# Performance work log

Measured on AMD Instinct MI355X. Metric: run time of the kernel, lower is better.

## Reference

```python
import jax, jax.numpy as jnp
import numpy as np

NG, NC, FG, FC, D = 8192, 4096, 512, 256, 64
ALPHA = 0.2          # leaky_relu negative slope
NEG = -9.0e15        # mask fill value from the torch code


def _leaky(x):
    return jnp.where(x >= 0, x, ALPHA * x)


def _relation(h_src, h_dst, a, adj):
    # additive GAT score: e[i,j] = leaky(h_src[i]@a[:D] + h_dst[j]@a[D:])
    s1 = h_src @ a[:D]            # [Ns]
    s2 = h_dst @ a[D:]            # [Nd]
    e = _leaky(s1[:, None] + s2[None, :])          # [Ns, Nd]
    att = jax.nn.softmax(jnp.where(adj > 0, e, NEG), axis=1)
    return att @ h_dst            # [Ns, D]


def setup_inputs() -> dict:
    key = jax.random.key(0)
    ks = jax.random.split(key, 14)
    sc = 0.05
    return {
        "gene_x": jax.random.normal(ks[0], (NG, FG), jnp.float32),
        "cell_x": jax.random.normal(ks[1], (NC, FC), jnp.float32),
        "W_g": jax.random.normal(ks[2], (FG, D), jnp.float32) * sc,
        "W_c": jax.random.normal(ks[3], (FC, D), jnp.float32) * sc,
        "a_gg": jax.random.normal(ks[4], (2 * D,), jnp.float32) * sc,
        "a_gc": jax.random.normal(ks[5], (2 * D,), jnp.float32) * sc,
        "a_cc": jax.random.normal(ks[6], (2 * D,), jnp.float32) * sc,
        "a_cg": jax.random.normal(ks[7], (2 * D,), jnp.float32) * sc,
        "Wgate_g": jax.random.normal(ks[8], (D, 1), jnp.float32) * sc,
        "bgate_g": jnp.full((1,), -2.0, jnp.float32),
        "Wgate_c": jax.random.normal(ks[9], (D, 1), jnp.float32) * sc,
        "bgate_c": jnp.full((1,), -2.0, jnp.float32),
        "gene_adj": jax.random.randint(ks[10], (NG, NG), 0, 2, jnp.int32),
        "cell_adj": jax.random.randint(ks[11], (NC, NC), 0, 2, jnp.int32),
        "gene_cell_adj": jax.random.randint(ks[12], (NG, NC), 0, 2, jnp.int32),
    }


def reference(gene_x, cell_x, W_g, W_c, a_gg, a_gc, a_cc, a_cg,
              Wgate_g, bgate_g, Wgate_c, bgate_c,
              gene_adj, cell_adj, gene_cell_adj):
    gene_h = gene_x @ W_g                              # [NG, D]
    cell_h = cell_x @ W_c                              # [NC, D]

    gene_from_gene = _relation(gene_h, gene_h, a_gg, gene_adj)
    gene_from_cell = _relation(gene_h, cell_h, a_gc, gene_cell_adj)
    cell_from_cell = _relation(cell_h, cell_h, a_cc, cell_adj)
    cell_from_gene = _relation(cell_h, gene_h, a_cg, gene_cell_adj.T)

    gamma_g = jax.nn.sigmoid(gene_h @ Wgate_g + bgate_g)   # [NG, 1]
    gamma_c = jax.nn.sigmoid(cell_h @ Wgate_c + bgate_c)   # [NC, 1]

    gene_out = _leaky(gene_h + gene_from_gene + gamma_g * gene_from_cell)
    cell_out = _leaky(cell_h + cell_from_cell + gamma_c * cell_from_gene)
    return gene_out, cell_out
```

## Files before the change

### kernel.cpp

```cpp
#include <hip/hip_runtime.h>

#define NG 8192
#define NC 4096
#define FG 512
#define FC 256
#define ALPHA 0.2f

typedef float f32x4 __attribute__((ext_vector_type(4)));
typedef short bf16x8 __attribute__((ext_vector_type(8)));

static __device__ __forceinline__ float leakyf(float x) { return fmaxf(x, ALPHA * x); }

static __device__ __forceinline__ unsigned short f2bf(float f) {
    unsigned u = __builtin_bit_cast(unsigned, f);
    u += 0x7fffu + ((u >> 16) & 1u);
    return (unsigned short)(u >> 16);
}

static __device__ __forceinline__ float wred(float v) {
#pragma unroll
    for (int m = 1; m < 64; m <<= 1) v += __shfl_xor(v, m, 64);
    return v;
}

__global__ __launch_bounds__(256) void pack_all(
    const int* __restrict__ gene_adj, const int* __restrict__ cell_adj,
    const int* __restrict__ gc_adj,
    unsigned char* __restrict__ bmGG, unsigned char* __restrict__ bmCC,
    unsigned char* __restrict__ bmGC)
{
    const int wave = threadIdx.x >> 6, lane = threadIdx.x & 63;
    const int r = blockIdx.x * 4 + wave;
    const int* row; unsigned char* brow; int C;
    if (r < NG)           { row = gene_adj + (size_t)r * NG;              brow = bmGG + (size_t)r * (NG >> 3);              C = NG; }
    else if (r < NG + NC) { int rr = r - NG;      row = cell_adj + (size_t)rr * NC; brow = bmCC + (size_t)rr * (NC >> 3); C = NC; }
    else                  { int rr = r - NG - NC; row = gc_adj   + (size_t)rr * NC; brow = bmGC + (size_t)rr * (NC >> 3); C = NC; }
    for (int j = lane * 8; j < C; j += 512) {
        int4 a0 = *(const int4*)(row + j);
        int4 a1 = *(const int4*)(row + j + 4);
        unsigned b = (unsigned)(a0.x > 0)        | ((unsigned)(a0.y > 0) << 1)
                   | ((unsigned)(a0.z > 0) << 2) | ((unsigned)(a0.w > 0) << 3)
                   | ((unsigned)(a1.x > 0) << 4) | ((unsigned)(a1.y > 0) << 5)
                   | ((unsigned)(a1.z > 0) << 6) | ((unsigned)(a1.w > 0) << 7);
        brow[j >> 3] = (unsigned char)b;
    }
}

static __device__ __forceinline__ void proj_body(
    const float* __restrict__ x, const float* __restrict__ W, int K, int N,
    float* __restrict__ h, unsigned short* __restrict__ hT,
    const float* __restrict__ aA, const float* __restrict__ aB,
    const float* __restrict__ aC, const float* __restrict__ aD,
    const float* __restrict__ aG, const float* __restrict__ bG,
    float* __restrict__ sA, float* __restrict__ sB, float* __restrict__ sC,
    float* __restrict__ sD, float* __restrict__ gam, int blk)
{
    const int wave = threadIdx.x >> 6, lane = threadIdx.x & 63;
    const int r0 = blk * 16 + wave * 4;
    const float* xr = x + (size_t)r0 * K;
    float acc0 = 0.f, acc1 = 0.f, acc2 = 0.f, acc3 = 0.f;
    for (int k = 0; k < K; k += 4) {
        float4 x0 = *(const float4*)(xr + k);
        float4 x1 = *(const float4*)(xr + K + k);
        float4 x2 = *(const float4*)(xr + 2 * (size_t)K + k);
        float4 x3 = *(const float4*)(xr + 3 * (size_t)K + k);
        float w0 = W[(k + 0) * 64 + lane];
        float w1 = W[(k + 1) * 64 + lane];
        float w2 = W[(k + 2) * 64 + lane];
        float w3 = W[(k + 3) * 64 + lane];
        acc0 += x0.x * w0 + x0.y * w1 + x0.z * w2 + x0.w * w3;
        acc1 += x1.x * w0 + x1.y * w1 + x1.z * w2 + x1.w * w3;
        acc2 += x2.x * w0 + x2.y * w1 + x2.z * w2 + x2.w * w3;
        acc3 += x3.x * w0 + x3.y * w1 + x3.z * w2 + x3.w * w3;
    }
    float accs[4] = {acc0, acc1, acc2, acc3};
    unsigned short hb[4];
#pragma unroll
    for (int t = 0; t < 4; t++) {
        h[(size_t)(r0 + t) * 64 + lane] = accs[t];
        hb[t] = f2bf(accs[t]);
    }
    *(ushort4*)&hT[(size_t)lane * N + r0] = make_ushort4(hb[0], hb[1], hb[2], hb[3]);

    const float cA = aA[lane], cB = aB[lane], cC = aC[lane], cD = aD[lane], cG = aG[lane];
    const float bias = bG[0];
#pragma unroll
    for (int t = 0; t < 4; t++) {
        float vA = wred(accs[t] * cA);
        float vB = wred(accs[t] * cB);
        float vC = wred(accs[t] * cC);
        float vD = wred(accs[t] * cD);
        float vG = wred(accs[t] * cG);
        if (lane == 0) {
            sA[r0 + t] = vA; sB[r0 + t] = vB; sC[r0 + t] = vC; sD[r0 + t] = vD;
            gam[r0 + t] = 1.f / (1.f + __expf(-(vG + bias)));
        }
    }
}

__global__ __launch_bounds__(256) void proj_all(
    const float* __restrict__ gene_x, const float* __restrict__ W_g,
    const float* __restrict__ cell_x, const float* __restrict__ W_c,
    float* __restrict__ gene_h, unsigned short* __restrict__ gene_hT,
    float* __restrict__ cell_h, unsigned short* __restrict__ cell_hT,
    const float* __restrict__ a_gg, const float* __restrict__ a_gc,
    const float* __restrict__ a_cc, const float* __restrict__ a_cg,
    const float* __restrict__ Wgg, const float* __restrict__ bgg,
    const float* __restrict__ Wgc, const float* __restrict__ bgc,
    float* s1gg, float* s2gg, float* s1gc, float* s2cg, float* gamg,
    float* s1cc, float* s2cc, float* s2gc, float* s1cg, float* gamc)
{
    if (blockIdx.x < NG / 16)
        proj_body(gene_x, W_g, FG, NG, gene_h, gene_hT,
                  a_gg, a_gg + 64, a_gc, a_cg + 64, Wgg, bgg,
                  s1gg, s2gg, s1gc, s2cg, gamg, blockIdx.x);
    else
        proj_body(cell_x, W_c, FC, NC, cell_h, cell_hT,
                  a_cc, a_cc + 64, a_gc + 64, a_cg, Wgc, bgc,
                  s1cc, s2cc, s2gc, s1cg, gamc, blockIdx.x - NG / 16);
}

static __device__ __forceinline__ void rel_row_nb(
    const unsigned char* __restrict__ bm, int bm_ld,
    const float* __restrict__ s1, const float* __restrict__ s2,
    const unsigned short* __restrict__ hT, int Nd,
    float* __restrict__ num, float* __restrict__ lsum, int Ns, int JS,
    int strip, int p)
{
    const int wave = threadIdx.x >> 6, lane = threadIdx.x & 63;
    const int m = lane & 15, kp = lane >> 4;
    const int jlen = Nd / JS, jbase = p * jlen;
    const int i_row = strip * 64 + wave * 16 + m;
    const float s1v = s1[i_row];
    const unsigned char* bmrow = bm + (size_t)i_row * bm_ld;
    const unsigned short* hb0 = hT + (size_t)(0 * 16 + m) * Nd;
    const unsigned short* hb1 = hT + (size_t)(1 * 16 + m) * Nd;
    const unsigned short* hb2 = hT + (size_t)(2 * 16 + m) * Nd;
    const unsigned short* hb3 = hT + (size_t)(3 * 16 + m) * Nd;
    f32x4 acc0 = {0.f, 0.f, 0.f, 0.f}, acc1 = acc0, acc2 = acc0, acc3 = acc0;
    float lacc = 0.f;
    const int NGRP = jlen >> 5;
#pragma unroll 2
    for (int g = 0; g < NGRP; ++g) {
        const int jg = jbase + g * 32 + kp * 8;
        unsigned byte = bmrow[jg >> 3];
        float4 sa = *(const float4*)&s2[jg];
        float4 sb = *(const float4*)&s2[jg + 4];
        bf16x8 b0 = *(const bf16x8*)&hb0[jg];
        bf16x8 b1 = *(const bf16x8*)&hb1[jg];
        bf16x8 b2 = *(const bf16x8*)&hb2[jg];
        bf16x8 b3 = *(const bf16x8*)&hb3[jg];
        float s2v[8] = {sa.x, sa.y, sa.z, sa.w, sb.x, sb.y, sb.z, sb.w};
        bf16x8 af;
#pragma unroll
        for (int t = 0; t < 8; t++) {
            float e = s1v + s2v[t];
            float w = ((byte >> t) & 1u) ? __expf(leakyf(e)) : 0.f;
            lacc += w;
            af[t] = (short)f2bf(w);
        }
        acc0 = __builtin_amdgcn_mfma_f32_16x16x32_bf16(af, b0, acc0, 0, 0, 0);
        acc1 = __builtin_amdgcn_mfma_f32_16x16x32_bf16(af, b1, acc1, 0, 0, 0);
        acc2 = __builtin_amdgcn_mfma_f32_16x16x32_bf16(af, b2, acc2, 0, 0, 0);
        acc3 = __builtin_amdgcn_mfma_f32_16x16x32_bf16(af, b3, acc3, 0, 0, 0);
    }
    const int orow0 = strip * 64 + wave * 16 + kp * 4;
#pragma unroll
    for (int r = 0; r < 4; r++) {
        size_t base = ((size_t)p * Ns + orow0 + r) * 64;
        num[base + m]      = acc0[r];
        num[base + 16 + m] = acc1[r];
        num[base + 32 + m] = acc2[r];
        num[base + 48 + m] = acc3[r];
    }
    lacc += __shfl_xor(lacc, 16, 64);
    lacc += __shfl_xor(lacc, 32, 64);
    if (kp == 0) lsum[(size_t)p * Ns + strip * 64 + wave * 16 + m] = lacc;
}

static __device__ __forceinline__ void rel_col_nb(
    const unsigned char* __restrict__ bm, int bm_ld,
    const float* __restrict__ s1, const float* __restrict__ s2,
    const unsigned short* __restrict__ hT, int Nd,
    float* __restrict__ num, float* __restrict__ lsum, int Ns, int JS,
    int strip, int p)
{
    const int wave = threadIdx.x >> 6, lane = threadIdx.x & 63;
    const int m = lane & 15, kp = lane >> 4;
    const int jlen = Nd / JS, jbase = p * jlen;
    const int i_row = strip * 64 + wave * 16 + m;
    const float s1v = s1[i_row];
    const int bcol = i_row >> 3, bbit = i_row & 7;
    const unsigned short* hb0 = hT + (size_t)(0 * 16 + m) * Nd;
    const unsigned short* hb1 = hT + (size_t)(1 * 16 + m) * Nd;
    const unsigned short* hb2 = hT + (size_t)(2 * 16 + m) * Nd;
    const unsigned short* hb3 = hT + (size_t)(3 * 16 + m) * Nd;
    f32x4 acc0 = {0.f, 0.f, 0.f, 0.f}, acc1 = acc0, acc2 = acc0, acc3 = acc0;
    float lacc = 0.f;
    const int NGRP = jlen >> 5;
#pragma unroll 2
    for (int g = 0; g < NGRP; ++g) {
        const int jg = jbase + g * 32 + kp * 8;
        const unsigned char* bp = bm + (size_t)jg * bm_ld + bcol;
        unsigned char by[8];
#pragma unroll
        for (int t = 0; t < 8; t++) by[t] = bp[(size_t)t * bm_ld];
        float4 sa = *(const float4*)&s2[jg];
        float4 sb = *(const float4*)&s2[jg + 4];
        bf16x8 b0 = *(const bf16x8*)&hb0[jg];
        bf16x8 b1 = *(const bf16x8*)&hb1[jg];
        bf16x8 b2 = *(const bf16x8*)&hb2[jg];
        bf16x8 b3 = *(const bf16x8*)&hb3[jg];
        float s2v[8] = {sa.x, sa.y, sa.z, sa.w, sb.x, sb.y, sb.z, sb.w};
        bf16x8 af;
#pragma unroll
        for (int t = 0; t < 8; t++) {
            float e = s1v + s2v[t];
            float w = ((by[t] >> bbit) & 1u) ? __expf(leakyf(e)) : 0.f;
            lacc += w;
            af[t] = (short)f2bf(w);
        }
        acc0 = __builtin_amdgcn_mfma_f32_16x16x32_bf16(af, b0, acc0, 0, 0, 0);
        acc1 = __builtin_amdgcn_mfma_f32_16x16x32_bf16(af, b1, acc1, 0, 0, 0);
        acc2 = __builtin_amdgcn_mfma_f32_16x16x32_bf16(af, b2, acc2, 0, 0, 0);
        acc3 = __builtin_amdgcn_mfma_f32_16x16x32_bf16(af, b3, acc3, 0, 0, 0);
    }
    const int orow0 = strip * 64 + wave * 16 + kp * 4;
#pragma unroll
    for (int r = 0; r < 4; r++) {
        size_t base = ((size_t)p * Ns + orow0 + r) * 64;
        num[base + m]      = acc0[r];
        num[base + 16 + m] = acc1[r];
        num[base + 32 + m] = acc2[r];
        num[base + 48 + m] = acc3[r];
    }
    lacc += __shfl_xor(lacc, 16, 64);
    lacc += __shfl_xor(lacc, 32, 64);
    if (kp == 0) lsum[(size_t)p * Ns + strip * 64 + wave * 16 + m] = lacc;
}

__global__ __launch_bounds__(256, 4) void rel_fused(
    const unsigned char* __restrict__ bmGG, const unsigned char* __restrict__ bmCC,
    const unsigned char* __restrict__ bmGC,
    const float* __restrict__ s1gg, const float* __restrict__ s2gg,
    const float* __restrict__ s1cc, const float* __restrict__ s2cc,
    const float* __restrict__ s1gc, const float* __restrict__ s2gc,
    const float* __restrict__ s1cg, const float* __restrict__ s2cg,
    const unsigned short* __restrict__ gene_hT, const unsigned short* __restrict__ cell_hT,
    float* __restrict__ numGG, float* __restrict__ lGG,
    float* __restrict__ numCC, float* __restrict__ lCC,
    float* __restrict__ numGC, float* __restrict__ lGC,
    float* __restrict__ numCG, float* __restrict__ lCG)
{
    const int b = blockIdx.x, rel = b >> 9, w = b & 511;
    if (rel == 0)
        rel_row_nb(bmGG, NG / 8, s1gg, s2gg, gene_hT, NG, numGG, lGG, NG, 4, w >> 2, w & 3);
    else if (rel == 1)
        rel_row_nb(bmCC, NC / 8, s1cc, s2cc, cell_hT, NC, numCC, lCC, NC, 8, w >> 3, w & 7);
    else if (rel == 2)
        rel_row_nb(bmGC, NC / 8, s1gc, s2gc, cell_hT, NC, numGC, lGC, NG, 4, w >> 2, w & 3);
    else
        rel_col_nb(bmGC, NC / 8, s1cg, s2cg, gene_hT, NG, numCG, lCG, NC, 8, w >> 3, w & 7);
}

static __device__ __forceinline__ void combine_body(
    const float* __restrict__ numS, const float* __restrict__ lS, int JSS,
    const float* __restrict__ numX, const float* __restrict__ lX, int JSX,
    int Ns, const float* __restrict__ h, const float* __restrict__ gam,
    float* __restrict__ out, int blk)
{
    int idx = blk * 256 + threadIdx.x;
    int i = idx >> 6, c = idx & 63;
    float nS = 0.f, dS = 0.f, nX = 0.f, dX = 0.f;
    for (int p = 0; p < JSS; p++) {
        nS += numS[((size_t)p * Ns + i) * 64 + c];
        dS += lS[(size_t)p * Ns + i];
    }
    for (int p = 0; p < JSX; p++) {
        nX += numX[((size_t)p * Ns + i) * 64 + c];
        dX += lX[(size_t)p * Ns + i];
    }
    float v = h[idx] + nS / dS + gam[i] * (nX / dX);
    out[idx] = leakyf(v);
}

__global__ __launch_bounds__(256) void combine_all(
    const float* __restrict__ numGG, const float* __restrict__ lGG,
    const float* __restrict__ numGC, const float* __restrict__ lGC,
    const float* __restrict__ numCC, const float* __restrict__ lCC,
    const float* __restrict__ numCG, const float* __restrict__ lCG,
    const float* __restrict__ gene_h, const float* __restrict__ cell_h,
    const float* __restrict__ gamg, const float* __restrict__ gamc,
    float* __restrict__ out_gene, float* __restrict__ out_cell)
{
    if (blockIdx.x < NG * 64 / 256)
        combine_body(numGG, lGG, 4, numGC, lGC, 4, NG, gene_h, gamg, out_gene, blockIdx.x);
    else
        combine_body(numCC, lCC, 8, numCG, lCG, 8, NC, cell_h, gamc, out_cell,
                     blockIdx.x - NG * 64 / 256);
}

extern "C" void kernel_launch(void* const* d_in, const int* in_sizes, int n_in,
                              void* d_out, int out_size, void* d_ws, size_t ws_size,
                              hipStream_t stream)
{
    const float* gene_x = (const float*)d_in[0];
    const float* cell_x = (const float*)d_in[1];
    const float* W_g    = (const float*)d_in[2];
    const float* W_c    = (const float*)d_in[3];
    const float* a_gg   = (const float*)d_in[4];
    const float* a_gc   = (const float*)d_in[5];
    const float* a_cc   = (const float*)d_in[6];
    const float* a_cg   = (const float*)d_in[7];
    const float* Wgg    = (const float*)d_in[8];
    const float* bgg    = (const float*)d_in[9];
    const float* Wgc    = (const float*)d_in[10];
    const float* bgc    = (const float*)d_in[11];
    const int* gene_adj = (const int*)d_in[12];
    const int* cell_adj = (const int*)d_in[13];
    const int* gc_adj   = (const int*)d_in[14];

    size_t off = 0;
    char* wsb = (char*)d_ws;
    auto alloc = [&](size_t bytes) -> void* {
        void* p = wsb + off;
        off += (bytes + 255) & ~(size_t)255;
        return p;
    };
    const int JS_GG = 4, JS_CC = 8, JS_GC = 4, JS_CG = 8;

    float* gene_h = (float*)alloc((size_t)NG * 64 * 4);
    float* cell_h = (float*)alloc((size_t)NC * 64 * 4);
    unsigned short* gene_hT = (unsigned short*)alloc((size_t)NG * 64 * 2);
    unsigned short* cell_hT = (unsigned short*)alloc((size_t)NC * 64 * 2);
    unsigned char* bmGG = (unsigned char*)alloc((size_t)NG * (NG / 8));
    unsigned char* bmCC = (unsigned char*)alloc((size_t)NC * (NC / 8));
    unsigned char* bmGC = (unsigned char*)alloc((size_t)NG * (NC / 8));
    float* s1gg = (float*)alloc(NG * 4);
    float* s2gg = (float*)alloc(NG * 4);
    float* s1gc = (float*)alloc(NG * 4);
    float* s2cg = (float*)alloc(NG * 4);
    float* gamg = (float*)alloc(NG * 4);
    float* s1cc = (float*)alloc(NC * 4);
    float* s2cc = (float*)alloc(NC * 4);
    float* s2gc = (float*)alloc(NC * 4);
    float* s1cg = (float*)alloc(NC * 4);
    float* gamc = (float*)alloc(NC * 4);
    float* numGG = (float*)alloc((size_t)NG * 64 * JS_GG * 4);
    float* lGG   = (float*)alloc((size_t)NG * JS_GG * 4);
    float* numGC = (float*)alloc((size_t)NG * 64 * JS_GC * 4);
    float* lGC   = (float*)alloc((size_t)NG * JS_GC * 4);
    float* numCC = (float*)alloc((size_t)NC * 64 * JS_CC * 4);
    float* lCC   = (float*)alloc((size_t)NC * JS_CC * 4);
    float* numCG = (float*)alloc((size_t)NC * 64 * JS_CG * 4);
    float* lCG   = (float*)alloc((size_t)NC * JS_CG * 4);

    float* out_gene = (float*)d_out;
    float* out_cell = (float*)d_out + (size_t)NG * 64;

    pack_all<<<(NG + NC + NG) / 4, 256, 0, stream>>>(gene_adj, cell_adj, gc_adj,
        bmGG, bmCC, bmGC);

    proj_all<<<NG / 16 + NC / 16, 256, 0, stream>>>(
        gene_x, W_g, cell_x, W_c, gene_h, gene_hT, cell_h, cell_hT,
        a_gg, a_gc, a_cc, a_cg, Wgg, bgg, Wgc, bgc,
        s1gg, s2gg, s1gc, s2cg, gamg, s1cc, s2cc, s2gc, s1cg, gamc);

    rel_fused<<<2048, 256, 0, stream>>>(bmGG, bmCC, bmGC,
        s1gg, s2gg, s1cc, s2cc, s1gc, s2gc, s1cg, s2cg,
        gene_hT, cell_hT,
        numGG, lGG, numCC, lCC, numGC, lGC, numCG, lCG);

    combine_all<<<(NG + NC) * 64 / 256, 256, 0, stream>>>(
        numGG, lGG, numGC, lGC, numCC, lCC, numCG, lCG,
        gene_h, cell_h, gamg, gamc, out_gene, out_cell);
}
```

Baseline: 743.0 us.

## Stage hT tiles in LDS, fuse pack+proj, compute row sums via MFMA

```diff
diff --git a/kernel.cpp b/kernel.cpp
--- a/kernel.cpp
+++ b/kernel.cpp
@@ -17,34 +17,19 @@
     return (unsigned short)(u >> 16);
 }
 
+static __device__ __forceinline__ unsigned pack2bf(float lo, float hi) {
+    return __builtin_amdgcn_perm(__builtin_bit_cast(unsigned, hi),
+                                 __builtin_bit_cast(unsigned, lo), 0x07060302u);
+}
+
 static __device__ __forceinline__ float wred(float v) {
 #pragma unroll
     for (int m = 1; m < 64; m <<= 1) v += __shfl_xor(v, m, 64);
     return v;
 }
 
-__global__ __launch_bounds__(256) void pack_all(
-    const int* __restrict__ gene_adj, const int* __restrict__ cell_adj,
-    const int* __restrict__ gc_adj,
-    unsigned char* __restrict__ bmGG, unsigned char* __restrict__ bmCC,
-    unsigned char* __restrict__ bmGC)
-{
-    const int wave = threadIdx.x >> 6, lane = threadIdx.x & 63;
-    const int r = blockIdx.x * 4 + wave;
-    const int* row; unsigned char* brow; int C;
-    if (r < NG)           { row = gene_adj + (size_t)r * NG;              brow = bmGG + (size_t)r * (NG >> 3);              C = NG; }
-    else if (r < NG + NC) { int rr = r - NG;      row = cell_adj + (size_t)rr * NC; brow = bmCC + (size_t)rr * (NC >> 3); C = NC; }
-    else                  { int rr = r - NG - NC; row = gc_adj   + (size_t)rr * NC; brow = bmGC + (size_t)rr * (NC >> 3); C = NC; }
-    for (int j = lane * 8; j < C; j += 512) {
-        int4 a0 = *(const int4*)(row + j);
-        int4 a1 = *(const int4*)(row + j + 4);
-        unsigned b = (unsigned)(a0.x > 0)        | ((unsigned)(a0.y > 0) << 1)
-                   | ((unsigned)(a0.z > 0) << 2) | ((unsigned)(a0.w > 0) << 3)
-                   | ((unsigned)(a1.x > 0) << 4) | ((unsigned)(a1.y > 0) << 5)
-                   | ((unsigned)(a1.z > 0) << 6) | ((unsigned)(a1.w > 0) << 7);
-        brow[j >> 3] = (unsigned char)b;
-    }
-}
+#define PACK_BLKS ((NG + NC + NG) / 4)
+#define PROJ_BLKS (NG / 16 + NC / 16)
 
 static __device__ __forceinline__ void proj_body(
     const float* __restrict__ x, const float* __restrict__ W, int K, int N,
@@ -98,7 +83,11 @@
     }
 }
 
-__global__ __launch_bounds__(256) void proj_all(
+__global__ __launch_bounds__(256) void prep_all(
+    const int* __restrict__ gene_adj, const int* __restrict__ cell_adj,
+    const int* __restrict__ gc_adj,
+    unsigned char* __restrict__ bmGG, unsigned char* __restrict__ bmCC,
+    unsigned char* __restrict__ bmGC,
     const float* __restrict__ gene_x, const float* __restrict__ W_g,
     const float* __restrict__ cell_x, const float* __restrict__ W_c,
     float* __restrict__ gene_h, unsigned short* __restrict__ gene_hT,
@@ -110,17 +99,88 @@
     float* s1gg, float* s2gg, float* s1gc, float* s2cg, float* gamg,
     float* s1cc, float* s2cc, float* s2gc, float* s1cg, float* gamc)
 {
-    if (blockIdx.x < NG / 16)
-        proj_body(gene_x, W_g, FG, NG, gene_h, gene_hT,
-                  a_gg, a_gg + 64, a_gc, a_cg + 64, Wgg, bgg,
-                  s1gg, s2gg, s1gc, s2cg, gamg, blockIdx.x);
-    else
-        proj_body(cell_x, W_c, FC, NC, cell_h, cell_hT,
-                  a_cc, a_cc + 64, a_gc + 64, a_cg, Wgc, bgc,
-                  s1cc, s2cc, s2gc, s1cg, gamc, blockIdx.x - NG / 16);
-}
-
-static __device__ __forceinline__ void rel_row_nb(
+    if (blockIdx.x < PACK_BLKS) {
+        const int wave = threadIdx.x >> 6, lane = threadIdx.x & 63;
+        const int r = blockIdx.x * 4 + wave;
+        const int* row; unsigned char* brow; int C;
+        if (r < NG)           { row = gene_adj + (size_t)r * NG;              brow = bmGG + (size_t)r * (NG >> 3);              C = NG; }
+        else if (r < NG + NC) { int rr = r - NG;      row = cell_adj + (size_t)rr * NC; brow = bmCC + (size_t)rr * (NC >> 3); C = NC; }
+        else                  { int rr = r - NG - NC; row = gc_adj   + (size_t)rr * NC; brow = bmGC + (size_t)rr * (NC >> 3); C = NC; }
+        for (int j = lane * 8; j < C; j += 512) {
+            int4 a0 = *(const int4*)(row + j);
+            int4 a1 = *(const int4*)(row + j + 4);
+            unsigned b = (unsigned)(a0.x > 0)        | ((unsigned)(a0.y > 0) << 1)
+                       | ((unsigned)(a0.z > 0) << 2) | ((unsigned)(a0.w > 0) << 3)
+                       | ((unsigned)(a1.x > 0) << 4) | ((unsigned)(a1.y > 0) << 5)
+                       | ((unsigned)(a1.z > 0) << 6) | ((unsigned)(a1.w > 0) << 7);
+            brow[j >> 3] = (unsigned char)b;
+        }
+    } else {
+        int blk = blockIdx.x - PACK_BLKS;
+        if (blk < NG / 16)
+            proj_body(gene_x, W_g, FG, NG, gene_h, gene_hT,
+                      a_gg, a_gg + 64, a_gc, a_cg + 64, Wgg, bgg,
+                      s1gg, s2gg, s1gc, s2cg, gamg, blk);
+        else
+            proj_body(cell_x, W_c, FC, NC, cell_h, cell_hT,
+                      a_cc, a_cc + 64, a_gc + 64, a_cg, Wgc, bgc,
+                      s1cc, s2cc, s2gc, s1cg, gamc, blk - NG / 16);
+    }
+}
+
+static __device__ __forceinline__ void rel_chunk_compute(
+    const unsigned short* hbuf, const float* s2buf,
+    unsigned mask_words[8], float s1v, int m, int kp,
+    f32x4& acc0, f32x4& acc1, f32x4& acc2, f32x4& acc3, f32x4& acc4,
+    const bf16x8 bones)
+{
+#pragma unroll
+    for (int g = 0; g < 8; ++g) {
+        const int jl = g * 32 + kp * 8;
+        float4 sa = *(const float4*)&s2buf[jl];
+        float4 sb = *(const float4*)&s2buf[jl + 4];
+        unsigned byte = (mask_words[g] >> (kp * 8)) & 0xffu;
+        bf16x8 b0 = *(const bf16x8*)&hbuf[(0 * 16 + m) * 264 + jl];
+        bf16x8 b1 = *(const bf16x8*)&hbuf[(1 * 16 + m) * 264 + jl];
+        bf16x8 b2 = *(const bf16x8*)&hbuf[(2 * 16 + m) * 264 + jl];
+        bf16x8 b3 = *(const bf16x8*)&hbuf[(3 * 16 + m) * 264 + jl];
+        float s2v[8] = {sa.x, sa.y, sa.z, sa.w, sb.x, sb.y, sb.z, sb.w};
+        float w[8];
+#pragma unroll
+        for (int t = 0; t < 8; t++) {
+            float e = s1v + s2v[t];
+            w[t] = ((byte >> t) & 1u) ? __expf(leakyf(e)) : 0.f;
+        }
+        uint4 pk = {pack2bf(w[0], w[1]), pack2bf(w[2], w[3]),
+                    pack2bf(w[4], w[5]), pack2bf(w[6], w[7])};
+        bf16x8 af = __builtin_bit_cast(bf16x8, pk);
+        acc0 = __builtin_amdgcn_mfma_f32_16x16x32_bf16(af, b0, acc0, 0, 0, 0);
+        acc1 = __builtin_amdgcn_mfma_f32_16x16x32_bf16(af, b1, acc1, 0, 0, 0);
+        acc2 = __builtin_amdgcn_mfma_f32_16x16x32_bf16(af, b2, acc2, 0, 0, 0);
+        acc3 = __builtin_amdgcn_mfma_f32_16x16x32_bf16(af, b3, acc3, 0, 0, 0);
+        acc4 = __builtin_amdgcn_mfma_f32_16x16x32_bf16(af, bones, acc4, 0, 0, 0);
+    }
+}
+
+static __device__ __forceinline__ void rel_epilogue(
+    const f32x4& acc0, const f32x4& acc1, const f32x4& acc2, const f32x4& acc3,
+    const f32x4& acc4, float* __restrict__ num, float* __restrict__ lsum,
+    int Ns, int p, int strip, int wave, int m, int kp)
+{
+    const int orow0 = strip * 64 + wave * 16 + kp * 4;
+#pragma unroll
+    for (int r = 0; r < 4; r++) {
+        size_t base = ((size_t)p * Ns + orow0 + r) * 64;
+        num[base + m]      = acc0[r];
+        num[base + 16 + m] = acc1[r];
+        num[base + 32 + m] = acc2[r];
+        num[base + 48 + m] = acc3[r];
+        if (m == 0) lsum[(size_t)p * Ns + orow0 + r] = acc4[r];
+    }
+}
+
+static __device__ __forceinline__ void rel_row_body(
+    unsigned short* hbuf, float* s2buf,
     const unsigned char* __restrict__ bm, int bm_ld,
     const float* __restrict__ s1, const float* __restrict__ s2,
     const unsigned short* __restrict__ hT, int Nd,
@@ -133,52 +193,29 @@
     const int i_row = strip * 64 + wave * 16 + m;
     const float s1v = s1[i_row];
     const unsigned char* bmrow = bm + (size_t)i_row * bm_ld;
-    const unsigned short* hb0 = hT + (size_t)(0 * 16 + m) * Nd;
-    const unsigned short* hb1 = hT + (size_t)(1 * 16 + m) * Nd;
-    const unsigned short* hb2 = hT + (size_t)(2 * 16 + m) * Nd;
-    const unsigned short* hb3 = hT + (size_t)(3 * 16 + m) * Nd;
-    f32x4 acc0 = {0.f, 0.f, 0.f, 0.f}, acc1 = acc0, acc2 = acc0, acc3 = acc0;
-    float lacc = 0.f;
-    const int NGRP = jlen >> 5;
-#pragma unroll 2
-    for (int g = 0; g < NGRP; ++g) {
-        const int jg = jbase + g * 32 + kp * 8;
-        unsigned byte = bmrow[jg >> 3];
-        float4 sa = *(const float4*)&s2[jg];
-        float4 sb = *(const float4*)&s2[jg + 4];
-        bf16x8 b0 = *(const bf16x8*)&hb0[jg];
-        bf16x8 b1 = *(const bf16x8*)&hb1[jg];
-        bf16x8 b2 = *(const bf16x8*)&hb2[jg];
-        bf16x8 b3 = *(const bf16x8*)&hb3[jg];
-        float s2v[8] = {sa.x, sa.y, sa.z, sa.w, sb.x, sb.y, sb.z, sb.w};
-        bf16x8 af;
-#pragma unroll
-        for (int t = 0; t < 8; t++) {
-            float e = s1v + s2v[t];
-            float w = ((byte >> t) & 1u) ? __expf(leakyf(e)) : 0.f;
-            lacc += w;
-            af[t] = (short)f2bf(w);
-        }
-        acc0 = __builtin_amdgcn_mfma_f32_16x16x32_bf16(af, b0, acc0, 0, 0, 0);
-        acc1 = __builtin_amdgcn_mfma_f32_16x16x32_bf16(af, b1, acc1, 0, 0, 0);
-        acc2 = __builtin_amdgcn_mfma_f32_16x16x32_bf16(af, b2, acc2, 0, 0, 0);
-        acc3 = __builtin_amdgcn_mfma_f32_16x16x32_bf16(af, b3, acc3, 0, 0, 0);
-    }
-    const int orow0 = strip * 64 + wave * 16 + kp * 4;
-#pragma unroll
-    for (int r = 0; r < 4; r++) {
-        size_t base = ((size_t)p * Ns + orow0 + r) * 64;
-        num[base + m]      = acc0[r];
-        num[base + 16 + m] = acc1[r];
-        num[base + 32 + m] = acc2[r];
-        num[base + 48 + m] = acc3[r];
-    }
-    lacc += __shfl_xor(lacc, 16, 64);
-    lacc += __shfl_xor(lacc, 32, 64);
-    if (kp == 0) lsum[(size_t)p * Ns + strip * 64 + wave * 16 + m] = lacc;
-}
-
-static __device__ __forceinline__ void rel_col_nb(
+    bf16x8 bones;
+#pragma unroll
+    for (int t = 0; t < 8; t++) bones[t] = (short)0x3f80;
+    f32x4 acc0 = {0.f, 0.f, 0.f, 0.f}, acc1 = acc0, acc2 = acc0, acc3 = acc0, acc4 = acc0;
+
+    for (int jc = jbase; jc < jbase + jlen; jc += 256) {
+        uint4 q0 = *(const uint4*)(bmrow + (jc >> 3));
+        uint4 q1 = *(const uint4*)(bmrow + (jc >> 3) + 16);
+        for (int idx = threadIdx.x; idx < 2048; idx += 256) {
+            int c = idx >> 5, off = (idx & 31) * 8;
+            *(int4*)&hbuf[c * 264 + off] = *(const int4*)&hT[(size_t)c * Nd + jc + off];
+        }
+        s2buf[threadIdx.x] = s2[jc + threadIdx.x];
+        __syncthreads();
+        unsigned words[8] = {q0.x, q0.y, q0.z, q0.w, q1.x, q1.y, q1.z, q1.w};
+        rel_chunk_compute(hbuf, s2buf, words, s1v, m, kp, acc0, acc1, acc2, acc3, acc4, bones);
+        __syncthreads();
+    }
+    rel_epilogue(acc0, acc1, acc2, acc3, acc4, num, lsum, Ns, p, strip, wave, m, kp);
+}
+
+static __device__ __forceinline__ void rel_col_body(
+    unsigned short* hbuf, float* s2buf,
     const unsigned char* __restrict__ bm, int bm_ld,
     const float* __restrict__ s1, const float* __restrict__ s2,
     const unsigned short* __restrict__ hT, int Nd,
@@ -191,52 +228,52 @@
     const int i_row = strip * 64 + wave * 16 + m;
     const float s1v = s1[i_row];
     const int bcol = i_row >> 3, bbit = i_row & 7;
-    const unsigned short* hb0 = hT + (size_t)(0 * 16 + m) * Nd;
-    const unsigned short* hb1 = hT + (size_t)(1 * 16 + m) * Nd;
-    const unsigned short* hb2 = hT + (size_t)(2 * 16 + m) * Nd;
-    const unsigned short* hb3 = hT + (size_t)(3 * 16 + m) * Nd;
-    f32x4 acc0 = {0.f, 0.f, 0.f, 0.f}, acc1 = acc0, acc2 = acc0, acc3 = acc0;
-    float lacc = 0.f;
-    const int NGRP = jlen >> 5;
-#pragma unroll 2
-    for (int g = 0; g < NGRP; ++g) {
-        const int jg = jbase + g * 32 + kp * 8;
-        const unsigned char* bp = bm + (size_t)jg * bm_ld + bcol;
-        unsigned char by[8];
-#pragma unroll
-        for (int t = 0; t < 8; t++) by[t] = bp[(size_t)t * bm_ld];
-        float4 sa = *(const float4*)&s2[jg];
-        float4 sb = *(const float4*)&s2[jg + 4];
-        bf16x8 b0 = *(const bf16x8*)&hb0[jg];
-        bf16x8 b1 = *(const bf16x8*)&hb1[jg];
-        bf16x8 b2 = *(const bf16x8*)&hb2[jg];
-        bf16x8 b3 = *(const bf16x8*)&hb3[jg];
-        float s2v[8] = {sa.x, sa.y, sa.z, sa.w, sb.x, sb.y, sb.z, sb.w};
-        bf16x8 af;
-#pragma unroll
-        for (int t = 0; t < 8; t++) {
-            float e = s1v + s2v[t];
-            float w = ((by[t] >> bbit) & 1u) ? __expf(leakyf(e)) : 0.f;
-            lacc += w;
-            af[t] = (short)f2bf(w);
-        }
-        acc0 = __builtin_amdgcn_mfma_f32_16x16x32_bf16(af, b0, acc0, 0, 0, 0);
-        acc1 = __builtin_amdgcn_mfma_f32_16x16x32_bf16(af, b1, acc1, 0, 0, 0);
-        acc2 = __builtin_amdgcn_mfma_f32_16x16x32_bf16(af, b2, acc2, 0, 0, 0);
-        acc3 = __builtin_amdgcn_mfma_f32_16x16x32_bf16(af, b3, acc3, 0, 0, 0);
-    }
-    const int orow0 = strip * 64 + wave * 16 + kp * 4;
-#pragma unroll
-    for (int r = 0; r < 4; r++) {
-        size_t base = ((size_t)p * Ns + orow0 + r) * 64;
-        num[base + m]      = acc0[r];
-        num[base + 16 + m] = acc1[r];
-        num[base + 32 + m] = acc2[r];
-        num[base + 48 + m] = acc3[r];
-    }
-    lacc += __shfl_xor(lacc, 16, 64);
-    lacc += __shfl_xor(lacc, 32, 64);
-    if (kp == 0) lsum[(size_t)p * Ns + strip * 64 + wave * 16 + m] = lacc;
+    bf16x8 bones;
+#pragma unroll
+    for (int t = 0; t < 8; t++) bones[t] = (short)0x3f80;
+    f32x4 acc0 = {0.f, 0.f, 0.f, 0.f}, acc1 = acc0, acc2 = acc0, acc3 = acc0, acc4 = acc0;
+
+    for (int jc = jbase; jc < jbase + jlen; jc += 256) {
+        for (int idx = threadIdx.x; idx < 2048; idx += 256) {
+            int c = idx >> 5, off = (idx & 31) * 8;
+            *(int4*)&hbuf[c * 264 + off] = *(const int4*)&hT[(size_t)c * Nd + jc + off];
+        }
+        s2buf[threadIdx.x] = s2[jc + threadIdx.x];
+        __syncthreads();
+#pragma unroll
+        for (int g = 0; g < 8; ++g) {
+            const int jl = g * 32 + kp * 8;
+            const int jg = jc + jl;
+            const unsigned char* bp = bm + (size_t)jg * bm_ld + bcol;
+            unsigned mw = 0;
+#pragma unroll
+            for (int t = 0; t < 8; t++)
+                mw |= ((unsigned)((bp[(size_t)t * bm_ld] >> bbit) & 1u)) << t;
+            float4 sa = *(const float4*)&s2buf[jl];
+            float4 sb = *(const float4*)&s2buf[jl + 4];
+            bf16x8 b0 = *(const bf16x8*)&hbuf[(0 * 16 + m) * 264 + jl];
+            bf16x8 b1 = *(const bf16x8*)&hbuf[(1 * 16 + m) * 264 + jl];
+            bf16x8 b2 = *(const bf16x8*)&hbuf[(2 * 16 + m) * 264 + jl];
+            bf16x8 b3 = *(const bf16x8*)&hbuf[(3 * 16 + m) * 264 + jl];
+            float s2v[8] = {sa.x, sa.y, sa.z, sa.w, sb.x, sb.y, sb.z, sb.w};
+            float w[8];
+#pragma unroll
+            for (int t = 0; t < 8; t++) {
+                float e = s1v + s2v[t];
+                w[t] = ((mw >> t) & 1u) ? __expf(leakyf(e)) : 0.f;
+            }
+            uint4 pk = {pack2bf(w[0], w[1]), pack2bf(w[2], w[3]),
+                        pack2bf(w[4], w[5]), pack2bf(w[6], w[7])};
+            bf16x8 af = __builtin_bit_cast(bf16x8, pk);
+            acc0 = __builtin_amdgcn_mfma_f32_16x16x32_bf16(af, b0, acc0, 0, 0, 0);
+            acc1 = __builtin_amdgcn_mfma_f32_16x16x32_bf16(af, b1, acc1, 0, 0, 0);
+            acc2 = __builtin_amdgcn_mfma_f32_16x16x32_bf16(af, b2, acc2, 0, 0, 0);
+            acc3 = __builtin_amdgcn_mfma_f32_16x16x32_bf16(af, b3, acc3, 0, 0, 0);
+            acc4 = __builtin_amdgcn_mfma_f32_16x16x32_bf16(af, bones, acc4, 0, 0, 0);
+        }
+        __syncthreads();
+    }
+    rel_epilogue(acc0, acc1, acc2, acc3, acc4, num, lsum, Ns, p, strip, wave, m, kp);
 }
 
 __global__ __launch_bounds__(256, 4) void rel_fused(
@@ -252,15 +289,26 @@
     float* __restrict__ numGC, float* __restrict__ lGC,
     float* __restrict__ numCG, float* __restrict__ lCG)
 {
-    const int b = blockIdx.x, rel = b >> 9, w = b & 511;
-    if (rel == 0)
-        rel_row_nb(bmGG, NG / 8, s1gg, s2gg, gene_hT, NG, numGG, lGG, NG, 4, w >> 2, w & 3);
-    else if (rel == 1)
-        rel_row_nb(bmCC, NC / 8, s1cc, s2cc, cell_hT, NC, numCC, lCC, NC, 8, w >> 3, w & 7);
-    else if (rel == 2)
-        rel_row_nb(bmGC, NC / 8, s1gc, s2gc, cell_hT, NC, numGC, lGC, NG, 4, w >> 2, w & 3);
-    else
-        rel_col_nb(bmGC, NC / 8, s1cg, s2cg, gene_hT, NG, numCG, lCG, NC, 8, w >> 3, w & 7);
+    __shared__ __align__(16) unsigned short hbuf[64 * 264];
+    __shared__ __align__(16) float s2buf[256];
+    const int b = blockIdx.x;
+    if (b < 1024) {
+        const int w = b;
+        rel_row_body(hbuf, s2buf, bmGG, NG / 8, s1gg, s2gg, gene_hT, NG,
+                     numGG, lGG, NG, 8, w >> 3, w & 7);
+    } else if (b < 1536) {
+        const int w = b - 1024;
+        rel_row_body(hbuf, s2buf, bmCC, NC / 8, s1cc, s2cc, cell_hT, NC,
+                     numCC, lCC, NC, 8, w >> 3, w & 7);
+    } else if (b < 2048) {
+        const int w = b - 1536;
+        rel_row_body(hbuf, s2buf, bmGC, NC / 8, s1gc, s2gc, cell_hT, NC,
+                     numGC, lGC, NG, 4, w >> 2, w & 3);
+    } else {
+        const int w = b - 2048;
+        rel_col_body(hbuf, s2buf, bmGC, NC / 8, s1cg, s2cg, gene_hT, NG,
+                     numCG, lCG, NC, 8, w >> 3, w & 7);
+    }
 }
 
 static __device__ __forceinline__ void combine_body(
@@ -294,7 +342,7 @@
     float* __restrict__ out_gene, float* __restrict__ out_cell)
 {
     if (blockIdx.x < NG * 64 / 256)
-        combine_body(numGG, lGG, 4, numGC, lGC, 4, NG, gene_h, gamg, out_gene, blockIdx.x);
+        combine_body(numGG, lGG, 8, numGC, lGC, 4, NG, gene_h, gamg, out_gene, blockIdx.x);
     else
         combine_body(numCC, lCC, 8, numCG, lCG, 8, NC, cell_h, gamc, out_cell,
                      blockIdx.x - NG * 64 / 256);
@@ -327,7 +375,7 @@
         off += (bytes + 255) & ~(size_t)255;
         return p;
     };
-    const int JS_GG = 4, JS_CC = 8, JS_GC = 4, JS_CG = 8;
+    const int JS_GG = 8, JS_CC = 8, JS_GC = 4, JS_CG = 8;
 
     float* gene_h = (float*)alloc((size_t)NG * 64 * 4);
     float* cell_h = (float*)alloc((size_t)NC * 64 * 4);
@@ -358,15 +406,13 @@
     float* out_gene = (float*)d_out;
     float* out_cell = (float*)d_out + (size_t)NG * 64;
 
-    pack_all<<<(NG + NC + NG) / 4, 256, 0, stream>>>(gene_adj, cell_adj, gc_adj,
-        bmGG, bmCC, bmGC);
-
-    proj_all<<<NG / 16 + NC / 16, 256, 0, stream>>>(
+    prep_all<<<PACK_BLKS + PROJ_BLKS, 256, 0, stream>>>(
+        gene_adj, cell_adj, gc_adj, bmGG, bmCC, bmGC,
         gene_x, W_g, cell_x, W_c, gene_h, gene_hT, cell_h, cell_hT,
         a_gg, a_gc, a_cc, a_cg, Wgg, bgg, Wgc, bgc,
         s1gg, s2gg, s1gc, s2cg, gamg, s1cc, s2cc, s2gc, s1cg, gamc);
 
-    rel_fused<<<2048, 256, 0, stream>>>(bmGG, bmCC, bmGC,
+    rel_fused<<<2560, 256, 0, stream>>>(bmGG, bmCC, bmGC,
         s1gg, s2gg, s1cc, s2cc, s1gc, s2gc, s1cg, s2cg,
         gene_hT, cell_hT,
         numGG, lGG, numCC, lCC, numGC, lGC, numCG, lCG);
```

Result: faster. 645.9 us (-13.1%).
